# Optimization experiments

Measured on AMD Instinct MI355X. Metric: run time of the kernel, lower is better.

The kernel has to match this reference:

```python
import jax, jax.numpy as jnp
import numpy as np

# Counts-based indexed grouped linear (canonical 'uv,u,v' path of
# SegmentedPolynomialIndexedLinear): tokens x[z] are sorted by group idx[z];
# output y[z] = coeff * x[z] @ W[idx[z]] where W = w.reshape(C, U, V).

C, U, V, Z = 8, 512, 512, 32768


def setup_inputs() -> dict:
    key = jax.random.key(0)
    kw, kx, ki = jax.random.split(key, 3)
    w = jax.random.normal(kw, (C, U * V), dtype=jnp.float32)  # [C, u*v] per-group weights
    x = jax.random.normal(kx, (Z, U), dtype=jnp.float32)      # [Z, u] tokens
    idx = jnp.sort(jax.random.randint(ki, (Z,), 0, C))        # sorted group ids (module asserts sortedness)
    coefficients = jnp.ones((1,), dtype=jnp.float32)          # path coefficient buffer
    return {"w": w, "x": x, "idx": idx, "coefficients": coefficients}


def reference(w, x, idx, coefficients):
    C_ = w.shape[0]
    Zt, U_ = x.shape
    V_ = w.shape[1] // U_
    Wg = w.reshape(C_, U_, V_)                                   # [C,u,v]
    # group membership (counts = bincount(idx) in the original; one-hot is its
    # dense, jit-friendly equivalent of the ragged grouped GEMM)
    onehot = (idx[:, None] == jnp.arange(C_)).astype(x.dtype)    # [Z,C]
    xg = jnp.einsum('zu,zc->czu', x, onehot)                     # [C,Z,u], zero outside own group
    y = jnp.einsum('czu,cuv->zv', xg, Wg)                        # [Z,v]
    return y * coefficients[0]
```

## Files before the change

kernel.cpp:

```cpp
#include <hip/hip_runtime.h>
#include <stdint.h>


#define Cg 8
#define Ud 512
#define Vd 512
#define Zd 32768

#define KT 16
#define NBN 2
#define NBM_MAX 519
#define GRID_GEMM (NBM_MAX * NBN)

#define WSW_US (Cg * 8 * KT * 4 * 512)
#define WS_NEEDED ((size_t)WSW_US * 2 + 64)

typedef __attribute__((ext_vector_type(8))) short bf16x8;
typedef __attribute__((ext_vector_type(4))) float f32x4;
typedef __attribute__((ext_vector_type(4))) unsigned short us4;
typedef __attribute__((ext_vector_type(4))) float float4v;
typedef __attribute__((ext_vector_type(4))) unsigned int u32x4;

__device__ __forceinline__ unsigned short f2bf(float f) {
    unsigned int u = __float_as_uint(f);
    u += 0x7fffu + ((u >> 16) & 1u);
    return (unsigned short)(u >> 16);
}
__device__ __forceinline__ unsigned int pk2(float lo, float hi) {
    return (unsigned int)f2bf(lo) | ((unsigned int)f2bf(hi) << 16);
}



__global__ __launch_bounds__(256)
void convert_w(const float* __restrict__ w, const int* __restrict__ idx,
               unsigned short* __restrict__ wsw, int* __restrict__ starts)
{
    const int t = blockIdx.x * 256 + threadIdx.x;
    const int g   = t >> 16;
    const int rem = t & 65535;
    const int u0  = (rem >> 9) << 2;
    const int v   = rem & 511;
    const float* src = w + ((size_t)g << 18) + (size_t)u0 * Vd + v;
    us4 p;
    p[0] = f2bf(src[0]);
    p[1] = f2bf(src[Vd]);
    p[2] = f2bf(src[2 * Vd]);
    p[3] = f2bf(src[3 * Vd]);
    const int vb = v >> 6, ct = (v >> 4) & 3, c = v & 15;
    const int kt = u0 >> 5;
    const int off = ((((g * 8 + vb) * KT + kt) * 4 + ct) << 9)
                  + (((u0 & 31) >> 3) << 7) + (c << 3) + (u0 & 7);
    *(us4*)(wsw + off) = p;

    if (blockIdx.x == 0 && threadIdx.x < 9) {
        const int gq = threadIdx.x;
        int lo = 0;
        if (gq >= 8) lo = Zd;
        else {
            int hi = Zd;
            while (lo < hi) { int mid = (lo + hi) >> 1;
                              if (idx[mid] < gq) lo = mid + 1; else hi = mid; }
        }
        starts[gq] = lo;
    }
}


__global__ __launch_bounds__(256, 2)
void sgl_gemm(const float* __restrict__ x,
              const unsigned short* __restrict__ wsw,
              const int* __restrict__ starts,
              const float* __restrict__ coeff,
              float* __restrict__ y)
{
    __shared__ unsigned short As[KT * 4 * 512];

    const int tid = threadIdx.x, lane = tid & 63, wave = tid >> 6;
    const int l15 = lane & 15, l4 = lane >> 4;

    const int bid = blockIdx.x;
    const int xcd = bid & 7, io = bid >> 3;
    const int wk  = (xcd < 6) ? xcd * 130 + io : 780 + (xcd - 6) * 129 + io;
    const int bmp = wk >> 1, bn = wk & 1;

    int s[9];
#pragma unroll
    for (int i = 0; i < 9; ++i) s[i] = starts[i];
    int g = -1, lblk = 0, ab = 0;
#pragma unroll
    for (int gg = 0; gg < 8; ++gg) {
        const int c  = s[gg + 1] - s[gg];
        const int nb = (c + 63) >> 6;
        if (g < 0 && bmp < ab + nb) { g = gg; lblk = bmp - ab; }
        ab += nb;
    }
    if (g < 0) return;
    const int start = s[g];
    const int cnt   = s[g + 1] - s[g];
    const int j0    = lblk << 6;

    const unsigned short* wV = wsw
        + ((size_t)((g * 8 + bn * 4 + wave) * KT) << 11);
    const int bfr = (l4 << 7) + (l15 << 3);

    const int sr  = tid >> 2;
    const int sk0 = (tid & 3) << 7;
    const int rc  = (j0 + sr < cnt) ? (j0 + sr) : (cnt - 1);
    const float* sx = x + (size_t)(start + rc) * Ud + sk0;
    const int awb = ((sr >> 4) << 9) + ((sr & 15) << 3);

#pragma unroll 4
    for (int j = 0; j < 16; ++j) {
        const int k0 = sk0 + j * 8;
        const float4v va = *(const float4v*)(sx + j * 8);
        const float4v vb2 = *(const float4v*)(sx + j * 8 + 4);
        u32x4 pw;
        pw[0] = pk2(va[0], va[1]);  pw[1] = pk2(va[2], va[3]);
        pw[2] = pk2(vb2[0], vb2[1]); pw[3] = pk2(vb2[2], vb2[3]);
        const int us = ((k0 >> 5) << 11) + awb + (((k0 & 31) >> 3) << 7);
        *(u32x4*)(&As[us]) = pw;
    }

    bf16x8 bp0[4], bp1[4];
#pragma unroll
    for (int ni = 0; ni < 4; ++ni)
        bp0[ni] = *(const bf16x8*)(wV + (ni << 9) + bfr);
#pragma unroll
    for (int ni = 0; ni < 4; ++ni)
        bp1[ni] = *(const bf16x8*)(wV + 2048 + (ni << 9) + bfr);

    f32x4 acc[4][4];
#pragma unroll
    for (int mi = 0; mi < 4; ++mi)
#pragma unroll
        for (int ni = 0; ni < 4; ++ni)
            acc[mi][ni] = f32x4{0.f, 0.f, 0.f, 0.f};

    asm volatile("s_waitcnt lgkmcnt(0)" ::: "memory");
    __builtin_amdgcn_s_barrier();

#pragma unroll
    for (int kt = 0; kt < KT; ++kt) {
        bf16x8 a_[4], bu[4];
#pragma unroll
        for (int mi = 0; mi < 4; ++mi)
            a_[mi] = *(const bf16x8*)(&As[(kt << 11) + (mi << 9) + bfr]);
#pragma unroll
        for (int ni = 0; ni < 4; ++ni)
            bu[ni] = (kt & 1) ? bp1[ni] : bp0[ni];
        if (kt + 2 < KT) {
            if (kt & 1) {
#pragma unroll
                for (int ni = 0; ni < 4; ++ni)
                    bp1[ni] = *(const bf16x8*)(wV + ((kt + 2) << 11) + (ni << 9) + bfr);
            } else {
#pragma unroll
                for (int ni = 0; ni < 4; ++ni)
                    bp0[ni] = *(const bf16x8*)(wV + ((kt + 2) << 11) + (ni << 9) + bfr);
            }
        }
#pragma unroll
        for (int mi = 0; mi < 4; ++mi)
#pragma unroll
            for (int ni = 0; ni < 4; ++ni)
                acc[mi][ni] = __builtin_amdgcn_mfma_f32_16x16x32_bf16(
                    a_[mi], bu[ni], acc[mi][ni], 0, 0, 0);
    }

    const float cf = coeff[0];
    const bool full = (j0 + 64) <= cnt;
#pragma unroll
    for (int mi = 0; mi < 4; ++mi) {
        const int rb = mi * 16 + l4 * 4;
#pragma unroll
        for (int ni = 0; ni < 4; ++ni) {
            const int c = bn * 256 + wave * 64 + ni * 16 + l15;
#pragma unroll
            for (int q = 0; q < 4; ++q) {
                if (full || (j0 + rb + q) < cnt)
                    y[(size_t)(start + j0 + rb + q) * Vd + c] = acc[mi][ni][q] * cf;
            }
        }
    }
}


__global__ __launch_bounds__(256)
void sgl_naive(const float* __restrict__ w, const float* __restrict__ x,
               const int* __restrict__ idx, const float* __restrict__ coeff,
               float* __restrict__ y)
{
    __shared__ float xs[Ud];
    const int z = blockIdx.x;
    const int g = idx[z];
    for (int u = threadIdx.x; u < Ud; u += 256) xs[u] = x[(size_t)z * Ud + u];
    __syncthreads();
    const float* Wg = w + (size_t)g * (Ud * Vd);
    const float cf = coeff[0];
    for (int v = threadIdx.x; v < Vd; v += 256) {
        float acc = 0.f;
        for (int u = 0; u < Ud; ++u) acc += xs[u] * Wg[(size_t)u * Vd + v];
        y[(size_t)z * Vd + v] = acc * cf;
    }
}

extern "C" void kernel_launch(void* const* d_in, const int* in_sizes, int n_in,
                              void* d_out, int out_size, void* d_ws, size_t ws_size,
                              hipStream_t stream) {
    const float* w     = (const float*)d_in[0];
    const float* x     = (const float*)d_in[1];
    const int*   idx   = (const int*)d_in[2];
    const float* coeff = (const float*)d_in[3];
    float* y = (float*)d_out;

    if (ws_size >= WS_NEEDED) {
        unsigned short* wsw = (unsigned short*)d_ws;
        int* starts = (int*)((char*)d_ws + (size_t)WSW_US * 2);
        hipLaunchKernelGGL(convert_w, dim3(2048), dim3(256), 0, stream,
                           w, idx, wsw, starts);
        hipLaunchKernelGGL(sgl_gemm, dim3(GRID_GEMM), dim3(256), 0, stream,
                           x, wsw, starts, coeff, y);
    } else {
        hipLaunchKernelGGL(sgl_naive, dim3(Zd), dim3(256), 0, stream,
                           w, x, idx, coeff, y);
    }
}
```

Before: 60.45 us.

## Retile grouped GEMM to 32-row blocks with 8 waves covering all columns

Switches the GEMM tile from 64 rows by 256 columns (two column blocks, 4 waves) to 32 rows by the full 512 columns with 8 waves per 512-thread block. x is staged once per row block instead of once per column half, and B fragments are prefetched three k-steps ahead in a rotating buffer. The XCD-aware block mapping is updated and the bf16 conversion now uses HIP intrinsics. Each wave still streams its whole B slice from global memory, and the smaller M tile halves the MFMA reuse of each B fragment, so weight traffic per output rises.

```diff
diff --git a/kernel.cpp b/kernel.cpp
--- a/kernel.cpp
+++ b/kernel.cpp
@@ -1,4 +1,5 @@
 #include <hip/hip_runtime.h>
+#include <hip/hip_bf16.h>
 #include <stdint.h>
 
 
@@ -8,9 +9,9 @@
 #define Zd 32768
 
 #define KT 16
-#define NBN 2
-#define NBM_MAX 519
-#define GRID_GEMM (NBM_MAX * NBN)
+#define BROW 32
+#define NBM_MAX 1031
+#define GRID_GEMM NBM_MAX
 
 #define WSW_US (Cg * 8 * KT * 4 * 512)
 #define WS_NEEDED ((size_t)WSW_US * 2 + 64)
@@ -21,15 +22,11 @@
 typedef __attribute__((ext_vector_type(4))) float float4v;
 typedef __attribute__((ext_vector_type(4))) unsigned int u32x4;
 
-__device__ __forceinline__ unsigned short f2bf(float f) {
-    unsigned int u = __float_as_uint(f);
-    u += 0x7fffu + ((u >> 16) & 1u);
-    return (unsigned short)(u >> 16);
-}
 __device__ __forceinline__ unsigned int pk2(float lo, float hi) {
-    return (unsigned int)f2bf(lo) | ((unsigned int)f2bf(hi) << 16);
-}
-
+    unsigned short l = __bfloat16_as_ushort(__float2bfloat16(lo));
+    unsigned short h = __bfloat16_as_ushort(__float2bfloat16(hi));
+    return (unsigned int)l | ((unsigned int)h << 16);
+}
 
 
 __global__ __launch_bounds__(256)
@@ -43,10 +40,10 @@
     const int v   = rem & 511;
     const float* src = w + ((size_t)g << 18) + (size_t)u0 * Vd + v;
     us4 p;
-    p[0] = f2bf(src[0]);
-    p[1] = f2bf(src[Vd]);
-    p[2] = f2bf(src[2 * Vd]);
-    p[3] = f2bf(src[3 * Vd]);
+    p[0] = (unsigned short)__bfloat16_as_ushort(__float2bfloat16(src[0]));
+    p[1] = (unsigned short)__bfloat16_as_ushort(__float2bfloat16(src[Vd]));
+    p[2] = (unsigned short)__bfloat16_as_ushort(__float2bfloat16(src[2 * Vd]));
+    p[3] = (unsigned short)__bfloat16_as_ushort(__float2bfloat16(src[3 * Vd]));
     const int vb = v >> 6, ct = (v >> 4) & 3, c = v & 15;
     const int kt = u0 >> 5;
     const int off = ((((g * 8 + vb) * KT + kt) * 4 + ct) << 9)
@@ -67,22 +64,41 @@
 }
 
 
-__global__ __launch_bounds__(256, 2)
+#define LDB(KTV, R) do {                                                      \
+    _Pragma("unroll")                                                         \
+    for (int ni_ = 0; ni_ < 4; ++ni_)                                         \
+        R[ni_] = *(const bf16x8*)(wV + ((KTV) << 11) + (ni_ << 9) + fr);      \
+  } while (0)
+
+#define CMPK(KTV, R) do {                                                     \
+    bf16x8 a_[2];                                                             \
+    a_[0] = *(const bf16x8*)(&As[((KTV) << 10) + fr]);                        \
+    a_[1] = *(const bf16x8*)(&As[((KTV) << 10) + 512 + fr]);                  \
+    _Pragma("unroll")                                                         \
+    for (int mi_ = 0; mi_ < 2; ++mi_)                                         \
+        _Pragma("unroll")                                                     \
+        for (int ni_ = 0; ni_ < 4; ++ni_)                                     \
+            acc[mi_][ni_] = __builtin_amdgcn_mfma_f32_16x16x32_bf16(          \
+                a_[mi_], R[ni_], acc[mi_][ni_], 0, 0, 0);                     \
+  } while (0)
+
+__global__ __launch_bounds__(512, 4)
 void sgl_gemm(const float* __restrict__ x,
               const unsigned short* __restrict__ wsw,
               const int* __restrict__ starts,
               const float* __restrict__ coeff,
               float* __restrict__ y)
 {
-    __shared__ unsigned short As[KT * 4 * 512];
+    __shared__ unsigned short As[KT * 1024];
 
     const int tid = threadIdx.x, lane = tid & 63, wave = tid >> 6;
     const int l15 = lane & 15, l4 = lane >> 4;
+    const int fr  = (l4 << 7) + (l15 << 3);
 
     const int bid = blockIdx.x;
     const int xcd = bid & 7, io = bid >> 3;
-    const int wk  = (xcd < 6) ? xcd * 130 + io : 780 + (xcd - 6) * 129 + io;
-    const int bmp = wk >> 1, bn = wk & 1;
+    const int wk  = (xcd < 7) ? xcd * 129 + io : 903 + io;
+    const int bmp = wk;
 
     int s[9];
 #pragma unroll
@@ -91,48 +107,50 @@
 #pragma unroll
     for (int gg = 0; gg < 8; ++gg) {
         const int c  = s[gg + 1] - s[gg];
-        const int nb = (c + 63) >> 6;
+        const int nb = (c + BROW - 1) >> 5;
         if (g < 0 && bmp < ab + nb) { g = gg; lblk = bmp - ab; }
         ab += nb;
     }
     if (g < 0) return;
     const int start = s[g];
     const int cnt   = s[g + 1] - s[g];
-    const int j0    = lblk << 6;
-
-    const unsigned short* wV = wsw
-        + ((size_t)((g * 8 + bn * 4 + wave) * KT) << 11);
-    const int bfr = (l4 << 7) + (l15 << 3);
-
-    const int sr  = tid >> 2;
-    const int sk0 = (tid & 3) << 7;
+    const int j0    = lblk << 5;
+
+    const int sr  = (tid >> 2) & 31;
+    const int sko = (tid & 3) << 3;
+    const int sk4 = tid >> 7;
     const int rc  = (j0 + sr < cnt) ? (j0 + sr) : (cnt - 1);
-    const float* sx = x + (size_t)(start + rc) * Ud + sk0;
-    const int awb = ((sr >> 4) << 9) + ((sr & 15) << 3);
-
-#pragma unroll 4
-    for (int j = 0; j < 16; ++j) {
-        const int k0 = sk0 + j * 8;
-        const float4v va = *(const float4v*)(sx + j * 8);
-        const float4v vb2 = *(const float4v*)(sx + j * 8 + 4);
+    const float* sx = x + (size_t)(start + rc) * Ud + sko;
+    const int swb = ((sr >> 4) << 9) + ((sko >> 3) << 7) + ((sr & 15) << 3);
+
+    float4v sv[4][2];
+#pragma unroll
+    for (int j = 0; j < 4; ++j) {
+        const int kt = 4 * j + sk4;
+        sv[j][0] = *(const float4v*)(sx + kt * 32);
+        sv[j][1] = *(const float4v*)(sx + kt * 32 + 4);
+    }
+
+    const unsigned short* wV = wsw + ((size_t)((g * 8 + wave) * KT) << 11);
+    bf16x8 B0[4], B1[4], B2[4];
+    LDB(0, B0);
+    LDB(1, B1);
+    LDB(2, B2);
+
+#pragma unroll
+    for (int j = 0; j < 4; ++j) {
+        const int kt = 4 * j + sk4;
         u32x4 pw;
-        pw[0] = pk2(va[0], va[1]);  pw[1] = pk2(va[2], va[3]);
-        pw[2] = pk2(vb2[0], vb2[1]); pw[3] = pk2(vb2[2], vb2[3]);
-        const int us = ((k0 >> 5) << 11) + awb + (((k0 & 31) >> 3) << 7);
-        *(u32x4*)(&As[us]) = pw;
-    }
-
-    bf16x8 bp0[4], bp1[4];
-#pragma unroll
-    for (int ni = 0; ni < 4; ++ni)
-        bp0[ni] = *(const bf16x8*)(wV + (ni << 9) + bfr);
-#pragma unroll
-    for (int ni = 0; ni < 4; ++ni)
-        bp1[ni] = *(const bf16x8*)(wV + 2048 + (ni << 9) + bfr);
-
-    f32x4 acc[4][4];
-#pragma unroll
-    for (int mi = 0; mi < 4; ++mi)
+        pw[0] = pk2(sv[j][0][0], sv[j][0][1]);
+        pw[1] = pk2(sv[j][0][2], sv[j][0][3]);
+        pw[2] = pk2(sv[j][1][0], sv[j][1][1]);
+        pw[3] = pk2(sv[j][1][2], sv[j][1][3]);
+        *(u32x4*)(&As[(kt << 10) + swb]) = pw;
+    }
+
+    f32x4 acc[2][4];
+#pragma unroll
+    for (int mi = 0; mi < 2; ++mi)
 #pragma unroll
         for (int ni = 0; ni < 4; ++ni)
             acc[mi][ni] = f32x4{0.f, 0.f, 0.f, 0.f};
@@ -142,40 +160,26 @@
 
 #pragma unroll
     for (int kt = 0; kt < KT; ++kt) {
-        bf16x8 a_[4], bu[4];
-#pragma unroll
-        for (int mi = 0; mi < 4; ++mi)
-            a_[mi] = *(const bf16x8*)(&As[(kt << 11) + (mi << 9) + bfr]);
-#pragma unroll
-        for (int ni = 0; ni < 4; ++ni)
-            bu[ni] = (kt & 1) ? bp1[ni] : bp0[ni];
-        if (kt + 2 < KT) {
-            if (kt & 1) {
-#pragma unroll
-                for (int ni = 0; ni < 4; ++ni)
-                    bp1[ni] = *(const bf16x8*)(wV + ((kt + 2) << 11) + (ni << 9) + bfr);
-            } else {
-#pragma unroll
-                for (int ni = 0; ni < 4; ++ni)
-                    bp0[ni] = *(const bf16x8*)(wV + ((kt + 2) << 11) + (ni << 9) + bfr);
-            }
+        if ((kt % 3) == 0) {
+            if (kt + 3 < KT) { CMPK(kt, B0); LDB(kt + 3, B0); }
+            else               CMPK(kt, B0);
+        } else if ((kt % 3) == 1) {
+            if (kt + 3 < KT) { CMPK(kt, B1); LDB(kt + 3, B1); }
+            else               CMPK(kt, B1);
+        } else {
+            if (kt + 3 < KT) { CMPK(kt, B2); LDB(kt + 3, B2); }
+            else               CMPK(kt, B2);
         }
-#pragma unroll
-        for (int mi = 0; mi < 4; ++mi)
-#pragma unroll
-            for (int ni = 0; ni < 4; ++ni)
-                acc[mi][ni] = __builtin_amdgcn_mfma_f32_16x16x32_bf16(
-                    a_[mi], bu[ni], acc[mi][ni], 0, 0, 0);
     }
 
     const float cf = coeff[0];
-    const bool full = (j0 + 64) <= cnt;
-#pragma unroll
-    for (int mi = 0; mi < 4; ++mi) {
+    const bool full = (j0 + BROW) <= cnt;
+#pragma unroll
+    for (int mi = 0; mi < 2; ++mi) {
         const int rb = mi * 16 + l4 * 4;
 #pragma unroll
         for (int ni = 0; ni < 4; ++ni) {
-            const int c = bn * 256 + wave * 64 + ni * 16 + l15;
+            const int c = wave * 64 + ni * 16 + l15;
 #pragma unroll
             for (int q = 0; q < 4; ++q) {
                 if (full || (j0 + rb + q) < cnt)
@@ -219,7 +223,7 @@
         int* starts = (int*)((char*)d_ws + (size_t)WSW_US * 2);
         hipLaunchKernelGGL(convert_w, dim3(2048), dim3(256), 0, stream,
                            w, idx, wsw, starts);
-        hipLaunchKernelGGL(sgl_gemm, dim3(GRID_GEMM), dim3(256), 0, stream,
+        hipLaunchKernelGGL(sgl_gemm, dim3(GRID_GEMM), dim3(512), 0, stream,
                            x, wsw, starts, coeff, y);
     } else {
         hipLaunchKernelGGL(sgl_naive, dim3(Zd), dim3(256), 0, stream,
```

Result: faster. 54.46 us (-9.9%).
